# Optimization experiments

Hardware: AMD Instinct MI355X
Metric: run time of the kernel (lower is better)

## Reference

```python
import jax, jax.numpy as jnp
import numpy as np

SCALE = 16.0 / 8  # alpha / rank

def setup_inputs() -> dict:
    key = jax.random.key(0)
    k1, k2, k3, k4 = jax.random.split(key, 4)
    B, S, D_IN, D_OUT, R = 4, 2048, 4096, 4096, 8
    x = jax.random.normal(k1, (B, S, D_IN), dtype=jnp.float32)
    weight = jax.random.normal(k2, (D_OUT, D_IN), dtype=jnp.float32) * (1.0 / np.sqrt(D_IN))
    lora_A = jax.random.normal(k3, (R, D_IN), dtype=jnp.float32) * (1.0 / np.sqrt(D_IN))
    lora_B = jax.random.normal(k4, (D_OUT, R), dtype=jnp.float32) * 0.01
    return {"x": x, "weight": weight, "lora_A": lora_A, "lora_B": lora_B}

def reference(x, weight, lora_A, lora_B):
    # base: x @ W^T  -> [B, S, out]
    base_out = jnp.einsum('bsd,od->bso', x, weight)
    # low-rank path, chained as (x @ A^T) @ B^T (same math as x @ (B@A)^T)
    xa = jnp.einsum('bsd,rd->bsr', x, lora_A)      # [B, S, r]
    lora_out = jnp.einsum('bsr,or->bso', xa, lora_B)  # [B, S, out]
    return base_out + SCALE * lora_out
```

## Files before the change

kernel.cpp:

```cpp
#include <hip/hip_runtime.h>
#include <hip/hip_bf16.h>

typedef unsigned short u16;
typedef __attribute__((ext_vector_type(8))) __bf16 bf16x8;
typedef __attribute__((ext_vector_type(4))) float f32x4;
typedef __attribute__((ext_vector_type(8))) unsigned short ushort8;

#define GM 8192
#define GN 4096
#define GK 4096
#define NT (GK / 64)

__device__ __forceinline__ u16 f2bf(float f) {
  unsigned u = __float_as_uint(f);
  u += 0x7fffu + ((u >> 16) & 1u);
  return (u16)(u >> 16);
}

__global__ void build_weff(const float* __restrict__ W,
                           const float* __restrict__ lA,
                           const float* __restrict__ lB,
                           u16* __restrict__ Weff) {
  const int o = blockIdx.x;
  float b[8];
#pragma unroll
  for (int r = 0; r < 8; ++r) b[r] = 2.0f * lB[o * 8 + r];
  const float* wrow = W + (size_t)o * GK;
  u16* orow = Weff + (size_t)o * GK;
  for (int d = threadIdx.x * 4; d < GK; d += blockDim.x * 4) {
    float4 w = *reinterpret_cast<const float4*>(wrow + d);
    float a0 = w.x, a1 = w.y, a2 = w.z, a3 = w.w;
#pragma unroll
    for (int r = 0; r < 8; ++r) {
      float4 a = *reinterpret_cast<const float4*>(lA + r * GK + d);
      a0 += b[r] * a.x; a1 += b[r] * a.y; a2 += b[r] * a.z; a3 += b[r] * a.w;
    }
    ushort4 p;
    p.x = f2bf(a0); p.y = f2bf(a1); p.z = f2bf(a2); p.w = f2bf(a3);
    *reinterpret_cast<ushort4*>(orow + d) = p;
  }
}

__global__ void cvt_bf16(const float* __restrict__ x, u16* __restrict__ xb) {
  const size_t i = ((size_t)blockIdx.x * blockDim.x + threadIdx.x) * 8;
  float4 v0 = *reinterpret_cast<const float4*>(x + i);
  float4 v1 = *reinterpret_cast<const float4*>(x + i + 4);
  ushort8 o;
  o[0] = f2bf(v0.x); o[1] = f2bf(v0.y); o[2] = f2bf(v0.z); o[3] = f2bf(v0.w);
  o[4] = f2bf(v1.x); o[5] = f2bf(v1.y); o[6] = f2bf(v1.z); o[7] = f2bf(v1.w);
  *reinterpret_cast<ushort8*>(xb + i) = o;
}

__device__ __forceinline__ void gload16(const u16* g, u16* l) {
  __builtin_amdgcn_global_load_lds(
      (const __attribute__((address_space(1))) void*)g,
      (__attribute__((address_space(3))) void*)l, 16, 0, 0);
}

#define BAR()                                  \
  do {                                         \
    asm volatile("" ::: "memory");             \
    __builtin_amdgcn_s_barrier();              \
    asm volatile("" ::: "memory");             \
  } while (0)

__global__ __launch_bounds__(512, 2) void gemm256(const u16* __restrict__ Ab,
                                                  const u16* __restrict__ Bb,
                                                  float* __restrict__ C) {
  __shared__ u16 lds[2][2][256 * 64];

  const int tid = threadIdx.x;
  const int wv = tid >> 6;
  const int l = tid & 63;

  const int nwg = gridDim.x;
  const int cpx = nwg >> 3;
  const int wg = ((int)blockIdx.x & 7) * cpx + ((int)blockIdx.x >> 3);
  const int tm = wg >> 4;
  const int tn = wg & 15;

  const int wr = wv >> 2;
  const int wc = wv & 3;

  const int srow = (wv << 3) + (l >> 3);
  const int srl = ((wv & 1) << 3) | (l >> 3);
  const int skel = ((l & 7) << 3) ^ ((srl & 0xE) << 2);
  const u16* aG = Ab + (size_t)(tm * 256) * GK;
  const u16* bG = Bb + (size_t)(tn * 256) * GK;

  const int frow = l & 15;
  const int fksw = ((l >> 4) << 3) ^ ((frow & 0xE) << 2);
  const int arow = wr * 128 + frow;
  const int brow = wc * 64 + frow;

  auto STAGE = [&](int th, int r) {
    const int k0 = th << 6;
    const u16* src = (r < 2 ? aG : bG) +
                     (size_t)((r & 1) * 128 + srow) * GK + k0 + skel;
    u16* dst = &lds[th & 1][r >> 1][(r & 1) * 8192 + wv * 512];
#pragma unroll
    for (int j = 0; j < 2; ++j)
      gload16(src + (size_t)(j * 64) * GK, dst + j * 4096);
  };

  STAGE(0, 0); STAGE(0, 1); STAGE(0, 2); STAGE(0, 3);
  STAGE(1, 2); STAGE(1, 0); STAGE(1, 1);

  f32x4 acc[8][4] = {};
  bf16x8 af[8][2], bfr[4][2];

  asm volatile("s_waitcnt vmcnt(6)" ::: "memory");
  BAR();

  for (int t = 0; t < NT; ++t) {
    const u16* A = &lds[t & 1][0][0];
    const u16* B = &lds[t & 1][1][0];
#pragma unroll
    for (int q = 0; q < 4; ++q) {
      if (q == 0) {
#pragma unroll
        for (int n = 0; n < 4; ++n)
#pragma unroll
          for (int s = 0; s < 2; ++s)
            bfr[n][s] = *reinterpret_cast<const bf16x8*>(
                B + (brow + n * 16) * 64 + (fksw ^ (s << 5)));
#pragma unroll
        for (int m = 0; m < 2; ++m)
#pragma unroll
          for (int s = 0; s < 2; ++s)
            af[m][s] = *reinterpret_cast<const bf16x8*>(
                A + (arow + m * 16) * 64 + (fksw ^ (s << 5)));
      } else if (q == 1) {
#pragma unroll
        for (int m = 2; m < 8; ++m)
#pragma unroll
          for (int s = 0; s < 2; ++s)
            af[m][s] = *reinterpret_cast<const bf16x8*>(
                A + (arow + m * 16) * 64 + (fksw ^ (s << 5)));
      }
      if (q == 0) { if (t + 1 < NT) STAGE(t + 1, 3); }
      else if (q == 1) { if (t + 2 < NT) STAGE(t + 2, 2); }
      else if (q == 2) { if (t + 2 < NT) STAGE(t + 2, 0); }
      else { if (t + 2 < NT) STAGE(t + 2, 1); }

      BAR();
      __builtin_amdgcn_s_setprio(1);
#pragma unroll
      for (int mm = 0; mm < 2; ++mm) {
#pragma unroll
        for (int n = 0; n < 4; ++n)
#pragma unroll
          for (int s = 0; s < 2; ++s)
            acc[2 * q + mm][n] = __builtin_amdgcn_mfma_f32_16x16x32_bf16(
                af[2 * q + mm][s], bfr[n][s], acc[2 * q + mm][n], 0, 0, 0);
      }
      __builtin_amdgcn_s_setprio(0);
      if (q == 3) {
        if (t < NT - 2)
          asm volatile("s_waitcnt vmcnt(6)" ::: "memory");
        else if (t == NT - 2)
          asm volatile("s_waitcnt vmcnt(0)" ::: "memory");
      }
      BAR();
    }
  }

  const int orow = tm * 256 + wr * 128 + ((l >> 4) << 2);
  const int ocol = tn * 256 + wc * 64 + (l & 15);
#pragma unroll
  for (int m = 0; m < 8; ++m)
#pragma unroll
    for (int n = 0; n < 4; ++n) {
      float* cp = C + (size_t)(orow + m * 16) * GN + (ocol + n * 16);
#pragma unroll
      for (int j = 0; j < 4; ++j) cp[(size_t)j * GN] = acc[m][n][j];
    }
}

extern "C" void kernel_launch(void* const* d_in, const int* in_sizes, int n_in,
                              void* d_out, int out_size, void* d_ws, size_t ws_size,
                              hipStream_t stream) {
  const float* x  = (const float*)d_in[0];
  const float* W  = (const float*)d_in[1];
  const float* lA = (const float*)d_in[2];
  const float* lB = (const float*)d_in[3];
  float* out = (float*)d_out;

  u16* weff = (u16*)d_ws;
  u16* xb = (u16*)((char*)d_ws + (size_t)GN * GK * sizeof(u16));

  build_weff<<<GN, 256, 0, stream>>>(W, lA, lB, weff);
  cvt_bf16<<<(size_t)GM * GK / (256 * 8), 256, 0, stream>>>(x, xb);
  gemm256<<<(GM / 256) * (GN / 256), 512, 0, stream>>>(xb, weff, out);
}
```

Baseline: 309.6 us.

## Restructure GEMM main loop into quadrant-wise register-prefetch ping-pong schedule

Replaces the 4-phase K-loop, which prefetched two tiles ahead, with a 2x-unrolled body. The body splits each 256x256 tile's MFMA work into four 4x2 quadrants and reads the next tile's A/B fragments into registers while the current quadrants compute. Global prefetch now runs only one tile ahead, with a full vmcnt(0) wait each iteration. The aim is to overlap LDS reads with MFMA more tightly and reduce register pressure. The trade-off is shallower global-load latency hiding.

Measured after the change: 575.4 us. +85.8%, slower.

```diff
diff --git a/kernel.cpp b/kernel.cpp
--- a/kernel.cpp
+++ b/kernel.cpp
@@ -103,66 +103,75 @@
       gload16(src + (size_t)(j * 64) * GK, dst + j * 4096);
   };
 
+  f32x4 acc[8][4] = {};
+  bf16x8 af_lo[4][2], af_hi[4][2], bfr1[2][2], b0A[2][2], b0B[2][2];
+
+#define RD_AF(dst, Abase, moff)                                        \
+  _Pragma("unroll") for (int m = 0; m < 4; ++m)                        \
+  _Pragma("unroll") for (int s = 0; s < 2; ++s)                        \
+      dst[m][s] = *reinterpret_cast<const bf16x8*>(                    \
+          (Abase) + (arow + (m + (moff)) * 16) * 64 + (fksw ^ (s << 5)));
+#define RD_B(dst, Bbase, noff)                                         \
+  _Pragma("unroll") for (int n = 0; n < 2; ++n)                        \
+  _Pragma("unroll") for (int s = 0; s < 2; ++s)                        \
+      dst[n][s] = *reinterpret_cast<const bf16x8*>(                    \
+          (Bbase) + (brow + (n + (noff)) * 16) * 64 + (fksw ^ (s << 5)));
+#define MFMA8(AF, BF, mo, no)                                          \
+  _Pragma("unroll") for (int m = 0; m < 4; ++m)                        \
+  _Pragma("unroll") for (int n = 0; n < 2; ++n)                        \
+  _Pragma("unroll") for (int s = 0; s < 2; ++s)                        \
+      acc[(mo) + m][(no) + n] = __builtin_amdgcn_mfma_f32_16x16x32_bf16( \
+          AF[m][s], BF[n][s], acc[(mo) + m][(no) + n], 0, 0, 0);
+
+#define BODY(T, ACUR, BCUR, ANXT, BNXT, OLDB, NEWB)                    \
+  {                                                                    \
+                                 \
+    RD_B(bfr1, BCUR, 2);                                               \
+    if ((T) + 1 < NT) STAGE((T) + 1, 0);                               \
+    BAR();                                                             \
+    __builtin_amdgcn_s_setprio(1);                                     \
+    MFMA8(af_lo, OLDB, 0, 0);                                          \
+    __builtin_amdgcn_s_setprio(0);                                     \
+    BAR();                                                             \
+                          \
+    RD_AF(af_hi, ACUR, 4);                                             \
+    if ((T) + 1 < NT) {                                                \
+      STAGE((T) + 1, 1); STAGE((T) + 1, 2); STAGE((T) + 1, 3);         \
+    }                                                                  \
+    BAR();                                                             \
+    __builtin_amdgcn_s_setprio(1);                                     \
+    MFMA8(af_lo, bfr1, 0, 2);                                          \
+    __builtin_amdgcn_s_setprio(0);                                     \
+    BAR();                                                             \
+     \
+    __builtin_amdgcn_s_setprio(1);                                     \
+    MFMA8(af_hi, bfr1, 4, 2);                                          \
+    __builtin_amdgcn_s_setprio(0);                                     \
+    asm volatile("s_waitcnt vmcnt(0)" ::: "memory");                   \
+    BAR();                                                             \
+                                 \
+    if ((T) + 1 < NT) {                                                \
+      RD_AF(af_lo, ANXT, 0);                                           \
+      RD_B(NEWB, BNXT, 0);                                             \
+    }                                                                  \
+    BAR();                                                             \
+    __builtin_amdgcn_s_setprio(1);                                     \
+    MFMA8(af_hi, OLDB, 4, 0);                                          \
+    __builtin_amdgcn_s_setprio(0);                                     \
+    BAR();                                                             \
+  }
+
   STAGE(0, 0); STAGE(0, 1); STAGE(0, 2); STAGE(0, 3);
-  STAGE(1, 2); STAGE(1, 0); STAGE(1, 1);
-
-  f32x4 acc[8][4] = {};
-  bf16x8 af[8][2], bfr[4][2];
-
-  asm volatile("s_waitcnt vmcnt(6)" ::: "memory");
+  asm volatile("s_waitcnt vmcnt(0)" ::: "memory");
   BAR();
-
-  for (int t = 0; t < NT; ++t) {
-    const u16* A = &lds[t & 1][0][0];
-    const u16* B = &lds[t & 1][1][0];
-#pragma unroll
-    for (int q = 0; q < 4; ++q) {
-      if (q == 0) {
-#pragma unroll
-        for (int n = 0; n < 4; ++n)
-#pragma unroll
-          for (int s = 0; s < 2; ++s)
-            bfr[n][s] = *reinterpret_cast<const bf16x8*>(
-                B + (brow + n * 16) * 64 + (fksw ^ (s << 5)));
-#pragma unroll
-        for (int m = 0; m < 2; ++m)
-#pragma unroll
-          for (int s = 0; s < 2; ++s)
-            af[m][s] = *reinterpret_cast<const bf16x8*>(
-                A + (arow + m * 16) * 64 + (fksw ^ (s << 5)));
-      } else if (q == 1) {
-#pragma unroll
-        for (int m = 2; m < 8; ++m)
-#pragma unroll
-          for (int s = 0; s < 2; ++s)
-            af[m][s] = *reinterpret_cast<const bf16x8*>(
-                A + (arow + m * 16) * 64 + (fksw ^ (s << 5)));
-      }
-      if (q == 0) { if (t + 1 < NT) STAGE(t + 1, 3); }
-      else if (q == 1) { if (t + 2 < NT) STAGE(t + 2, 2); }
-      else if (q == 2) { if (t + 2 < NT) STAGE(t + 2, 0); }
-      else { if (t + 2 < NT) STAGE(t + 2, 1); }
-
-      BAR();
-      __builtin_amdgcn_s_setprio(1);
-#pragma unroll
-      for (int mm = 0; mm < 2; ++mm) {
-#pragma unroll
-        for (int n = 0; n < 4; ++n)
-#pragma unroll
-          for (int s = 0; s < 2; ++s)
-            acc[2 * q + mm][n] = __builtin_amdgcn_mfma_f32_16x16x32_bf16(
-                af[2 * q + mm][s], bfr[n][s], acc[2 * q + mm][n], 0, 0, 0);
-      }
-      __builtin_amdgcn_s_setprio(0);
-      if (q == 3) {
-        if (t < NT - 2)
-          asm volatile("s_waitcnt vmcnt(6)" ::: "memory");
-        else if (t == NT - 2)
-          asm volatile("s_waitcnt vmcnt(0)" ::: "memory");
-      }
-      BAR();
-    }
+  RD_AF(af_lo, (&lds[0][0][0]), 0);
+  RD_B(b0A, (&lds[0][1][0]), 0);
+
+  for (int t = 0; t < NT; t += 2) {
+    BODY(t, (&lds[0][0][0]), (&lds[0][1][0]), (&lds[1][0][0]),
+         (&lds[1][1][0]), b0A, b0B);
+    BODY(t + 1, (&lds[1][0][0]), (&lds[1][1][0]), (&lds[0][0][0]),
+         (&lds[0][1][0]), b0B, b0A);
   }
 
   const int orow = tm * 256 + wr * 128 + ((l >> 4) << 2);
```

## Restructure GEMM main loop into 4-phase ping-pong with cross-iteration A-fragment prefetch

Applied to the files above, without the earlier changes.

Rewrites the GEMM inner loop as four explicit phases, each doing 16 MFMAs over a 4x2 sub-block. A fragments are split into lo and hi halves so the next tile's lo half is read from LDS during the current iteration. Out-of-range stage indices are clamped rather than branched on, so the vmcnt accounting stays uniform, at the cost of redundant trailing global loads. The aim is finer overlap of LDS reads, global-to-LDS loads and MFMA, with less idle time at barriers, but the hand-tuned waitcnt counts risk races if they are off.

New measurement: 293.5 us. -5.2%, faster.

```diff
diff --git a/kernel.cpp b/kernel.cpp
--- a/kernel.cpp
+++ b/kernel.cpp
@@ -94,7 +94,8 @@
   const int brow = wc * 64 + frow;
 
   auto STAGE = [&](int th, int r) {
-    const int k0 = th << 6;
+    const int tc = th < NT ? th : NT - 1;
+    const int k0 = tc << 6;
     const u16* src = (r < 2 ? aG : bG) +
                      (size_t)((r & 1) * 128 + srow) * GK + k0 + skel;
     u16* dst = &lds[th & 1][r >> 1][(r & 1) * 8192 + wv * 512];
@@ -103,66 +104,69 @@
       gload16(src + (size_t)(j * 64) * GK, dst + j * 4096);
   };
 
+  f32x4 acc[8][4] = {};
+  bf16x8 af_lo[4][2], af_hi[4][2], bfr[4][2];
+
+#define RD_AF(dst, Abase, moff)                                        \
+  _Pragma("unroll") for (int m = 0; m < 4; ++m)                        \
+  _Pragma("unroll") for (int s = 0; s < 2; ++s)                        \
+      dst[m][s] = *reinterpret_cast<const bf16x8*>(                    \
+          (Abase) + (arow + (m + (moff)) * 16) * 64 + (fksw ^ (s << 5)));
+#define RD_B2(n0, Bbase)                                               \
+  _Pragma("unroll") for (int n = 0; n < 2; ++n)                        \
+  _Pragma("unroll") for (int s = 0; s < 2; ++s)                        \
+      bfr[(n0) + n][s] = *reinterpret_cast<const bf16x8*>(             \
+          (Bbase) + (brow + ((n0) + n) * 16) * 64 + (fksw ^ (s << 5)));
+#define MFMA16(AF, nb, mo, no)                                         \
+  _Pragma("unroll") for (int m = 0; m < 4; ++m)                        \
+  _Pragma("unroll") for (int n = 0; n < 2; ++n)                        \
+  _Pragma("unroll") for (int s = 0; s < 2; ++s)                        \
+      acc[(mo) + m][(no) + n] = __builtin_amdgcn_mfma_f32_16x16x32_bf16( \
+          AF[m][s], bfr[(nb) + n][s], acc[(mo) + m][(no) + n], 0, 0, 0);
+
   STAGE(0, 0); STAGE(0, 1); STAGE(0, 2); STAGE(0, 3);
-  STAGE(1, 2); STAGE(1, 0); STAGE(1, 1);
-
-  f32x4 acc[8][4] = {};
-  bf16x8 af[8][2], bfr[4][2];
-
-  asm volatile("s_waitcnt vmcnt(6)" ::: "memory");
+  STAGE(1, 0); STAGE(1, 1); STAGE(1, 2);
+  asm volatile("s_waitcnt vmcnt(0)" ::: "memory");
   BAR();
+  RD_AF(af_lo, (&lds[0][0][0]), 0);
 
   for (int t = 0; t < NT; ++t) {
     const u16* A = &lds[t & 1][0][0];
     const u16* B = &lds[t & 1][1][0];
-#pragma unroll
-    for (int q = 0; q < 4; ++q) {
-      if (q == 0) {
-#pragma unroll
-        for (int n = 0; n < 4; ++n)
-#pragma unroll
-          for (int s = 0; s < 2; ++s)
-            bfr[n][s] = *reinterpret_cast<const bf16x8*>(
-                B + (brow + n * 16) * 64 + (fksw ^ (s << 5)));
-#pragma unroll
-        for (int m = 0; m < 2; ++m)
-#pragma unroll
-          for (int s = 0; s < 2; ++s)
-            af[m][s] = *reinterpret_cast<const bf16x8*>(
-                A + (arow + m * 16) * 64 + (fksw ^ (s << 5)));
-      } else if (q == 1) {
-#pragma unroll
-        for (int m = 2; m < 8; ++m)
-#pragma unroll
-          for (int s = 0; s < 2; ++s)
-            af[m][s] = *reinterpret_cast<const bf16x8*>(
-                A + (arow + m * 16) * 64 + (fksw ^ (s << 5)));
-      }
-      if (q == 0) { if (t + 1 < NT) STAGE(t + 1, 3); }
-      else if (q == 1) { if (t + 2 < NT) STAGE(t + 2, 2); }
-      else if (q == 2) { if (t + 2 < NT) STAGE(t + 2, 0); }
-      else { if (t + 2 < NT) STAGE(t + 2, 1); }
+    const u16* Anx = &lds[(t + 1) & 1][0][0];
 
-      BAR();
-      __builtin_amdgcn_s_setprio(1);
-#pragma unroll
-      for (int mm = 0; mm < 2; ++mm) {
-#pragma unroll
-        for (int n = 0; n < 4; ++n)
-#pragma unroll
-          for (int s = 0; s < 2; ++s)
-            acc[2 * q + mm][n] = __builtin_amdgcn_mfma_f32_16x16x32_bf16(
-                af[2 * q + mm][s], bfr[n][s], acc[2 * q + mm][n], 0, 0, 0);
-      }
-      __builtin_amdgcn_s_setprio(0);
-      if (q == 3) {
-        if (t < NT - 2)
-          asm volatile("s_waitcnt vmcnt(6)" ::: "memory");
-        else if (t == NT - 2)
-          asm volatile("s_waitcnt vmcnt(0)" ::: "memory");
-      }
-      BAR();
-    }
+    RD_B2(0, B);
+    RD_B2(2, B);
+    STAGE(t + 1, 3);
+    BAR();
+    asm volatile("s_waitcnt lgkmcnt(4)" ::: "memory");
+    __builtin_amdgcn_s_setprio(1);
+    MFMA16(af_lo, 0, 0, 0);
+    __builtin_amdgcn_s_setprio(0);
+
+    RD_AF(af_hi, A, 4);
+    STAGE(t + 2, 2);
+    asm volatile("s_waitcnt vmcnt(4)" ::: "memory");
+    BAR();
+    asm volatile("s_waitcnt lgkmcnt(8)" ::: "memory");
+    __builtin_amdgcn_s_setprio(1);
+    MFMA16(af_lo, 2, 0, 2);
+    __builtin_amdgcn_s_setprio(0);
+
+    RD_AF(af_lo, Anx, 0);
+    STAGE(t + 2, 0);
+    BAR();
+    asm volatile("s_waitcnt lgkmcnt(8)" ::: "memory");
+    __builtin_amdgcn_s_setprio(1);
+    MFMA16(af_hi, 2, 4, 2);
+    __builtin_amdgcn_s_setprio(0);
+
+    STAGE(t + 2, 1);
+    asm volatile("s_waitcnt vmcnt(6)" ::: "memory");
+    BAR();
+    __builtin_amdgcn_s_setprio(1);
+    MFMA16(af_hi, 0, 4, 0);
+    __builtin_amdgcn_s_setprio(0);
   }
 
   const int orow = tm * 256 + wr * 128 + ((l >> 4) << 2);
```

## Switch GEMM to 32x32x16 MFMA with a simpler single-stage prefetch loop

Applied to the files above, without the earlier changes.

Replaces the 16x16x32 bf16 MFMA tiling with 32x32x16 MFMA tiles, using 4x2 accumulators of 16 floats per wave and a matching fragment swizzle and output store mapping. The quarter-split main loop, with its two-tile-ahead prefetch and partial vmcnt waits, becomes a simpler one: wait for all loads, barrier, read every fragment for the tile, issue the next tile's copies, then run all MFMAs. Larger MFMA tiles cut LDS fragment reads per FLOP, but the shallower prefetch and the full vmcnt(0) wait each iteration may expose global-load latency.

Result: slower. 340.0 us (+9.8%).

```diff
diff --git a/kernel.cpp b/kernel.cpp
--- a/kernel.cpp
+++ b/kernel.cpp
@@ -3,7 +3,7 @@
 
 typedef unsigned short u16;
 typedef __attribute__((ext_vector_type(8))) __bf16 bf16x8;
-typedef __attribute__((ext_vector_type(4))) float f32x4;
+typedef __attribute__((ext_vector_type(16))) float f32x16;
 typedef __attribute__((ext_vector_type(8))) unsigned short ushort8;
 
 #define GM 8192
@@ -88,10 +88,10 @@
   const u16* aG = Ab + (size_t)(tm * 256) * GK;
   const u16* bG = Bb + (size_t)(tn * 256) * GK;
 
-  const int frow = l & 15;
-  const int fksw = ((l >> 4) << 3) ^ ((frow & 0xE) << 2);
-  const int arow = wr * 128 + frow;
-  const int brow = wc * 64 + frow;
+  const int fr32 = l & 31;
+  const int fksw = (((l >> 5) & 1) << 3) ^ ((l & 0xE) << 2);
+  const int arow = wr * 128 + fr32;
+  const int brow = wc * 64 + fr32;
 
   auto STAGE = [&](int th, int r) {
     const int k0 = th << 6;
@@ -104,76 +104,57 @@
   };
 
   STAGE(0, 0); STAGE(0, 1); STAGE(0, 2); STAGE(0, 3);
-  STAGE(1, 2); STAGE(1, 0); STAGE(1, 1);
 
-  f32x4 acc[8][4] = {};
-  bf16x8 af[8][2], bfr[4][2];
-
-  asm volatile("s_waitcnt vmcnt(6)" ::: "memory");
-  BAR();
+  f32x16 acc[4][2] = {};
+  bf16x8 af[4][4], bf[4][2];
 
   for (int t = 0; t < NT; ++t) {
+    asm volatile("s_waitcnt vmcnt(0)" ::: "memory");
+    BAR();
+
     const u16* A = &lds[t & 1][0][0];
     const u16* B = &lds[t & 1][1][0];
+
 #pragma unroll
-    for (int q = 0; q < 4; ++q) {
-      if (q == 0) {
+    for (int ks = 0; ks < 4; ++ks) {
 #pragma unroll
-        for (int n = 0; n < 4; ++n)
+      for (int nt = 0; nt < 2; ++nt)
+        bf[ks][nt] = *reinterpret_cast<const bf16x8*>(
+            B + (brow + nt * 32) * 64 + ((ks << 4) ^ fksw));
 #pragma unroll
-          for (int s = 0; s < 2; ++s)
-            bfr[n][s] = *reinterpret_cast<const bf16x8*>(
-                B + (brow + n * 16) * 64 + (fksw ^ (s << 5)));
+      for (int mt = 0; mt < 4; ++mt)
+        af[ks][mt] = *reinterpret_cast<const bf16x8*>(
+            A + (arow + mt * 32) * 64 + ((ks << 4) ^ fksw));
+    }
+
+    if (t + 1 < NT) {
+      STAGE(t + 1, 0); STAGE(t + 1, 1); STAGE(t + 1, 2); STAGE(t + 1, 3);
+    }
+
+    __builtin_amdgcn_s_setprio(1);
 #pragma unroll
-        for (int m = 0; m < 2; ++m)
+    for (int ks = 0; ks < 4; ++ks)
 #pragma unroll
-          for (int s = 0; s < 2; ++s)
-            af[m][s] = *reinterpret_cast<const bf16x8*>(
-                A + (arow + m * 16) * 64 + (fksw ^ (s << 5)));
-      } else if (q == 1) {
+      for (int mt = 0; mt < 4; ++mt)
 #pragma unroll
-        for (int m = 2; m < 8; ++m)
-#pragma unroll
-          for (int s = 0; s < 2; ++s)
-            af[m][s] = *reinterpret_cast<const bf16x8*>(
-                A + (arow + m * 16) * 64 + (fksw ^ (s << 5)));
-      }
-      if (q == 0) { if (t + 1 < NT) STAGE(t + 1, 3); }
-      else if (q == 1) { if (t + 2 < NT) STAGE(t + 2, 2); }
-      else if (q == 2) { if (t + 2 < NT) STAGE(t + 2, 0); }
-      else { if (t + 2 < NT) STAGE(t + 2, 1); }
-
-      BAR();
-      __builtin_amdgcn_s_setprio(1);
-#pragma unroll
-      for (int mm = 0; mm < 2; ++mm) {
-#pragma unroll
-        for (int n = 0; n < 4; ++n)
-#pragma unroll
-          for (int s = 0; s < 2; ++s)
-            acc[2 * q + mm][n] = __builtin_amdgcn_mfma_f32_16x16x32_bf16(
-                af[2 * q + mm][s], bfr[n][s], acc[2 * q + mm][n], 0, 0, 0);
-      }
-      __builtin_amdgcn_s_setprio(0);
-      if (q == 3) {
-        if (t < NT - 2)
-          asm volatile("s_waitcnt vmcnt(6)" ::: "memory");
-        else if (t == NT - 2)
-          asm volatile("s_waitcnt vmcnt(0)" ::: "memory");
-      }
-      BAR();
-    }
+        for (int nt = 0; nt < 2; ++nt)
+          acc[mt][nt] = __builtin_amdgcn_mfma_f32_32x32x16_bf16(
+              af[ks][mt], bf[ks][nt], acc[mt][nt], 0, 0, 0);
+    __builtin_amdgcn_s_setprio(0);
   }
 
-  const int orow = tm * 256 + wr * 128 + ((l >> 4) << 2);
-  const int ocol = tn * 256 + wc * 64 + (l & 15);
+  const int orow = tm * 256 + wr * 128 + 4 * (l >> 5);
+  const int ocol = tn * 256 + wc * 64 + (l & 31);
 #pragma unroll
-  for (int m = 0; m < 8; ++m)
+  for (int mt = 0; mt < 4; ++mt)
 #pragma unroll
-    for (int n = 0; n < 4; ++n) {
-      float* cp = C + (size_t)(orow + m * 16) * GN + (ocol + n * 16);
+    for (int nt = 0; nt < 2; ++nt) {
+      float* cp = C + (size_t)(orow + mt * 32) * GN + (ocol + nt * 32);
 #pragma unroll
-      for (int j = 0; j < 4; ++j) cp[(size_t)j * GN] = acc[m][n][j];
+      for (int j = 0; j < 16; ++j) {
+        const int rr = (j & 3) + 8 * (j >> 2);
+        cp[(size_t)rr * GN] = acc[mt][nt][j];
+      }
     }
 }
 
```
